# Optimization experiments

Measured on AMD Instinct MI355X. Metric: run time of the kernel, lower is better.

## Reference

```python
import jax, jax.numpy as jnp
import numpy as np
from jax import lax

DIL_R = 2            # dilation_radius
K = 2 * DIL_R + 1    # 5x5 morphology kernel
FOCAL_ALPHA = 0.25
FOCAL_GAMMA = 2.0
BOUNDARY_W = 1.0
IGNORE_IDX = 250


def setup_inputs() -> dict:
    key = jax.random.key(0)
    k1, k2 = jax.random.split(key)
    pred = jax.random.normal(k1, (32, 2, 512, 512), dtype=jnp.float32)
    target = jax.random.randint(k2, (32, 512, 512), 0, 2, dtype=jnp.int64)
    return {"pred": pred, "target": target}


def _boundary_mask(target):
    # labels float, 5x5 all-ones conv with 'same' padding (zero pad),
    # dilated = (conv > 0), eroded = (-conv(-x) > K*K-1) == (conv(x) > K*K-1)
    x = target.astype(jnp.float32)[:, None]                    # [B,1,H,W]
    kern = jnp.ones((1, 1, K, K), dtype=jnp.float32)
    s = lax.conv_general_dilated(x, kern, (1, 1), 'SAME',
                                 dimension_numbers=('NCHW', 'OIHW', 'NCHW'))
    dilated = (s > 0).astype(jnp.float32)
    eroded = (s > (K * K - 1)).astype(jnp.float32)
    return (dilated - eroded)[:, 0]                            # [B,H,W]


def _loss(pred, target, boundary):
    logp = jax.nn.log_softmax(pred, axis=1)                    # [B,2,H,W]
    # per-pixel CE
    ce_pix = -jnp.take_along_axis(logp, target[:, None].astype(jnp.int32), axis=1)[:, 0]  # [B,H,W]
    # main CE with ignore_index=250
    valid = (target != IGNORE_IDX)
    ce_loss = jnp.sum(ce_pix * valid) / jnp.maximum(jnp.sum(valid), 1)
    # focal loss (no ignore, mean over all pixels)
    pt = jnp.exp(-ce_pix)
    focal = jnp.mean(FOCAL_ALPHA * (1.0 - pt) ** FOCAL_GAMMA * ce_pix)
    # boundary dice on class-1 prob
    prob1 = jnp.exp(logp[:, 1])                                # softmax(pred,1)[:,1]
    tgt_f = target.astype(jnp.float32)
    bp = prob1 * boundary
    bt = tgt_f * boundary
    inter = jnp.sum(bp * bt, axis=(1, 2))
    union = jnp.sum(bp, axis=(1, 2)) + jnp.sum(bt, axis=(1, 2))
    dice = 2.0 * inter / (union + 1e-8)
    bdice = 1.0 - jnp.mean(dice)
    return ce_loss + BOUNDARY_W * focal + BOUNDARY_W * bdice


def reference(pred, target):
    boundary = _boundary_mask(target)
    return _loss(pred, target, boundary)
```

## Files before the change

### kernel.cpp

```cpp
#include <hip/hip_runtime.h>
#include <math.h>

#define BATCH 32
#define HH 512
#define WW 512
#define TH 16
#define HALO 2
#define SRH (TH + 2*HALO)
#define NDW (WW / 4)
#define CSTRIDE 132
#define NPIX ((float)BATCH * HH * WW)
#define HW (HH * WW)

#define SLOT(j,b) ((((j) * BATCH) + (b)) * 32)
#define WS_FLOATS (6 * BATCH * 32)

__global__ void zero_ws_kernel(float* ws) {
    int i = blockIdx.x * 256 + threadIdx.x;
    if (i < WS_FLOATS) ws[i] = 0.0f;
}

__global__ __launch_bounds__(256) void bel_main_kernel(
        const float* __restrict__ pred,
        const int*   __restrict__ target,
        float*       __restrict__ ws) {
    __shared__ unsigned int t8[SRH][NDW];
    __shared__ unsigned int csum[TH][CSTRIDE];
    __shared__ float red[6][4];

    const int tid = threadIdx.x;
    const int bid = blockIdx.x;
    const int b   = bid >> 5;
    const int ty  = bid & 31;
    const int y0  = ty * TH;
    const size_t tb = (size_t)b * HW;

    if (tid < 2 * TH) {
        int rr = tid >> 1;
        csum[rr][(tid & 1) ? (NDW + 1) : 0] = 0u;
    }

    #pragma unroll
    for (int it = 0; it < (SRH * NDW) / 256; ++it) {
        const int i  = tid + 256 * it;
        const int r  = i >> 7;
        const int c4 = i & 127;
        const int gy = y0 - HALO + r;
        unsigned int packed = 0u;
        if ((unsigned)gy < (unsigned)HH) {
            const int4 v = *(const int4*)(target + tb + ((size_t)gy << 9) + (c4 << 2));
            packed = (unsigned)v.x | ((unsigned)v.y << 8)
                   | ((unsigned)v.z << 16) | ((unsigned)v.w << 24);
        }
        t8[r][c4] = packed;
    }
    __syncthreads();

    #pragma unroll
    for (int it = 0; it < (TH * NDW) / 256; ++it) {
        const int j = tid + 256 * it;
        const int r = j >> 7;
        const int c = j & 127;
        csum[r][c + 1] = t8[r][c] + t8[r+1][c] + t8[r+2][c]
                       + t8[r+3][c] + t8[r+4][c];
    }
    __syncthreads();

    const float4* __restrict__ pr0 = (const float4*)(pred + tb * 2);
    const float4* __restrict__ pr1 = (const float4*)(pred + tb * 2 + HW);

    float ce_acc = 0.f, cnt_acc = 0.f, focal_acc = 0.f;
    float inter_acc = 0.f, bp_acc = 0.f, bt_acc = 0.f;

    const unsigned long long M5 = 0xFFFFFFFFFFull;
    const unsigned long long ALL5 = 0x0505050505ull;

    for (int it = 0; it < (TH * NDW) / 256; ++it) {
        const int j = tid + 256 * it;
        const int r = j >> 7;
        const int g = j & 127;
        const int y = y0 + r;
        const int fidx = (y << 7) + g;

        const float4 f0 = pr0[fidx];
        const float4 f1 = pr1[fidx];

        const unsigned int L = csum[r][g];
        const unsigned int M = csum[r][g + 1];
        const unsigned int R = csum[r][g + 2];
        const unsigned int tdw = t8[r + HALO][g];

        const unsigned long long lo  = (unsigned long long)L | ((unsigned long long)M << 32);
        const unsigned long long mid = (unsigned long long)M | ((unsigned long long)R << 32);

        #pragma unroll
        for (int i = 0; i < 4; ++i) {
            unsigned long long w;
            if      (i == 0) w = (lo  >> 16) & M5;
            else if (i == 1) w = (lo  >> 24) & M5;
            else if (i == 2) w =  mid        & M5;
            else             w = (mid >>  8) & M5;
            const float bm = (w != 0ull && w != ALL5) ? 1.0f : 0.0f;

            const unsigned int tv = (tdw >> (8 * i)) & 0xFFu;

            const float p0 = (i == 0) ? f0.x : (i == 1) ? f0.y : (i == 2) ? f0.z : f0.w;
            const float p1 = (i == 0) ? f1.x : (i == 1) ? f1.y : (i == 2) ? f1.z : f1.w;

            const float d  = p1 - p0;
            const float e  = __expf(-fabsf(d));
            const float rz = 1.0f / (1.0f + e);
            const float pmin = e * rz;
            const float prob1 = (d >= 0.0f) ? rz : pmin;
            const float pt = tv ? prob1 : (1.0f - prob1);
            const float ce = -__logf(pt);

            const float valid = (tv != 250u) ? 1.0f : 0.0f;
            ce_acc  += ce * valid;
            cnt_acc += valid;

            const float omp = 1.0f - pt;
            focal_acc += omp * omp * ce;

            const float bp = prob1 * bm;
            const float bt = (float)tv * bm;
            inter_acc += bp * bt;
            bp_acc    += bp;
            bt_acc    += bt;
        }
    }

    float vals[6] = {ce_acc, cnt_acc, focal_acc * 0.25f, inter_acc, bp_acc, bt_acc};
    #pragma unroll
    for (int jj = 0; jj < 6; ++jj) {
        float v = vals[jj];
        #pragma unroll
        for (int off = 32; off > 0; off >>= 1)
            v += __shfl_down(v, off, 64);
        vals[jj] = v;
    }
    const int wave = tid >> 6;
    const int lane = tid & 63;
    if (lane == 0) {
        #pragma unroll
        for (int jj = 0; jj < 6; ++jj) red[jj][wave] = vals[jj];
    }
    __syncthreads();
    if (tid == 0) {
        #pragma unroll
        for (int jj = 0; jj < 6; ++jj) {
            const float v = red[jj][0] + red[jj][1] + red[jj][2] + red[jj][3];
            atomicAdd(&ws[SLOT(jj, b)], v);
        }
    }
}

__global__ void bel_finalize_kernel(const float* __restrict__ ws,
                                    float* __restrict__ out) {
    const int t = threadIdx.x;
    float ce_p = 0.f, cnt_p = 0.f, focal_p = 0.f, dice_p = 0.f;
    if (t < BATCH) {
        ce_p    = ws[SLOT(0, t)];
        cnt_p   = ws[SLOT(1, t)];
        focal_p = ws[SLOT(2, t)];
        const float inter = ws[SLOT(3, t)];
        const float uni   = ws[SLOT(4, t)] + ws[SLOT(5, t)];
        dice_p = 2.0f * inter / (uni + 1e-8f);
    }
    #pragma unroll
    for (int off = 32; off > 0; off >>= 1) {
        ce_p    += __shfl_down(ce_p, off, 64);
        cnt_p   += __shfl_down(cnt_p, off, 64);
        focal_p += __shfl_down(focal_p, off, 64);
        dice_p  += __shfl_down(dice_p, off, 64);
    }
    if (t == 0) {
        const float ce_loss = ce_p / fmaxf(cnt_p, 1.0f);
        const float focal   = focal_p / NPIX;
        const float bdice   = 1.0f - dice_p / (float)BATCH;
        out[0] = ce_loss + focal + bdice;
    }
}

extern "C" void kernel_launch(void* const* d_in, const int* in_sizes, int n_in,
                              void* d_out, int out_size, void* d_ws, size_t ws_size,
                              hipStream_t stream) {
    const float* pred   = (const float*)d_in[0];
    const int*   target = (const int*)d_in[1];
    float* ws  = (float*)d_ws;
    float* out = (float*)d_out;

    zero_ws_kernel<<<(WS_FLOATS + 255) / 256, 256, 0, stream>>>(ws);
    bel_main_kernel<<<BATCH * (HH / TH), 256, 0, stream>>>(pred, target, ws);
    bel_finalize_kernel<<<1, 64, 0, stream>>>(ws, out);
}
```

Measured before the change: 118.7 us.

## Prefetch pred tile into registers and replace atomics with per-block partials

```diff
diff --git a/kernel.cpp b/kernel.cpp
--- a/kernel.cpp
+++ b/kernel.cpp
@@ -11,16 +11,10 @@
 #define CSTRIDE 132
 #define NPIX ((float)BATCH * HH * WW)
 #define HW (HH * WW)
-
-#define SLOT(j,b) ((((j) * BATCH) + (b)) * 32)
-#define WS_FLOATS (6 * BATCH * 32)
-
-__global__ void zero_ws_kernel(float* ws) {
-    int i = blockIdx.x * 256 + threadIdx.x;
-    if (i < WS_FLOATS) ws[i] = 0.0f;
-}
-
-__global__ __launch_bounds__(256) void bel_main_kernel(
+#define NBLK (BATCH * (HH / TH))
+
+
+__global__ __launch_bounds__(256, 4) void bel_main_kernel(
         const float* __restrict__ pred,
         const int*   __restrict__ target,
         float*       __restrict__ ws) {
@@ -68,6 +62,13 @@
 
     const float4* __restrict__ pr0 = (const float4*)(pred + tb * 2);
     const float4* __restrict__ pr1 = (const float4*)(pred + tb * 2 + HW);
+    const int base4 = (y0 << 7) + tid;
+
+    float4 F0[8], F1[8];
+    #pragma unroll
+    for (int it = 0; it < 8; ++it) F0[it] = pr0[base4 + 256 * it];
+    #pragma unroll
+    for (int it = 0; it < 8; ++it) F1[it] = pr1[base4 + 256 * it];
 
     float ce_acc = 0.f, cnt_acc = 0.f, focal_acc = 0.f;
     float inter_acc = 0.f, bp_acc = 0.f, bt_acc = 0.f;
@@ -75,15 +76,15 @@
     const unsigned long long M5 = 0xFFFFFFFFFFull;
     const unsigned long long ALL5 = 0x0505050505ull;
 
-    for (int it = 0; it < (TH * NDW) / 256; ++it) {
-        const int j = tid + 256 * it;
-        const int r = j >> 7;
-        const int g = j & 127;
-        const int y = y0 + r;
-        const int fidx = (y << 7) + g;
-
-        const float4 f0 = pr0[fidx];
-        const float4 f1 = pr1[fidx];
+    const int g  = tid & 127;
+    const int rb = tid >> 7;
+
+    #pragma unroll
+    for (int it = 0; it < 8; ++it) {
+        const int r = rb + 2 * it;
+
+        const float4 f0 = F0[it];
+        const float4 f1 = F1[it];
 
         const unsigned int L = csum[r][g];
         const unsigned int M = csum[r][g + 1];
@@ -147,38 +148,62 @@
     }
     __syncthreads();
     if (tid == 0) {
-        #pragma unroll
-        for (int jj = 0; jj < 6; ++jj) {
-            const float v = red[jj][0] + red[jj][1] + red[jj][2] + red[jj][3];
-            atomicAdd(&ws[SLOT(jj, b)], v);
-        }
+        float* p = ws + bid * 8;
+        #pragma unroll
+        for (int jj = 0; jj < 6; ++jj)
+            p[jj] = red[jj][0] + red[jj][1] + red[jj][2] + red[jj][3];
     }
 }
 
 __global__ void bel_finalize_kernel(const float* __restrict__ ws,
                                     float* __restrict__ out) {
+    __shared__ float simg[BATCH][4];
     const int t = threadIdx.x;
-    float ce_p = 0.f, cnt_p = 0.f, focal_p = 0.f, dice_p = 0.f;
+    const int b = t >> 3;
+    const int s = t & 7;
+
+    float a0 = 0.f, a1 = 0.f, a2 = 0.f, a3 = 0.f, a4 = 0.f, a5 = 0.f;
+    #pragma unroll
+    for (int k = 0; k < 4; ++k) {
+        const int bid = (b << 5) + s + (k << 3);
+        const float* p = ws + bid * 8;
+        a0 += p[0]; a1 += p[1]; a2 += p[2];
+        a3 += p[3]; a4 += p[4]; a5 += p[5];
+    }
+    #pragma unroll
+    for (int off = 4; off > 0; off >>= 1) {
+        a0 += __shfl_down(a0, off, 8);
+        a1 += __shfl_down(a1, off, 8);
+        a2 += __shfl_down(a2, off, 8);
+        a3 += __shfl_down(a3, off, 8);
+        a4 += __shfl_down(a4, off, 8);
+        a5 += __shfl_down(a5, off, 8);
+    }
+    if (s == 0) {
+        simg[b][0] = a0;
+        simg[b][1] = a1;
+        simg[b][2] = a2;
+        simg[b][3] = 2.0f * a3 / (a4 + a5 + 1e-8f);
+    }
+    __syncthreads();
     if (t < BATCH) {
-        ce_p    = ws[SLOT(0, t)];
-        cnt_p   = ws[SLOT(1, t)];
-        focal_p = ws[SLOT(2, t)];
-        const float inter = ws[SLOT(3, t)];
-        const float uni   = ws[SLOT(4, t)] + ws[SLOT(5, t)];
-        dice_p = 2.0f * inter / (uni + 1e-8f);
-    }
-    #pragma unroll
-    for (int off = 32; off > 0; off >>= 1) {
-        ce_p    += __shfl_down(ce_p, off, 64);
-        cnt_p   += __shfl_down(cnt_p, off, 64);
-        focal_p += __shfl_down(focal_p, off, 64);
-        dice_p  += __shfl_down(dice_p, off, 64);
-    }
-    if (t == 0) {
-        const float ce_loss = ce_p / fmaxf(cnt_p, 1.0f);
-        const float focal   = focal_p / NPIX;
-        const float bdice   = 1.0f - dice_p / (float)BATCH;
-        out[0] = ce_loss + focal + bdice;
+        float ce  = simg[t][0];
+        float cnt = simg[t][1];
+        float foc = simg[t][2];
+        float dc  = simg[t][3];
+        #pragma unroll
+        for (int off = 16; off > 0; off >>= 1) {
+            ce  += __shfl_down(ce,  off, 32);
+            cnt += __shfl_down(cnt, off, 32);
+            foc += __shfl_down(foc, off, 32);
+            dc  += __shfl_down(dc,  off, 32);
+        }
+        if (t == 0) {
+            const float ce_loss = ce / fmaxf(cnt, 1.0f);
+            const float focal   = foc / NPIX;
+            const float bdice   = 1.0f - dc / (float)BATCH;
+            out[0] = ce_loss + focal + bdice;
+        }
     }
 }
 
@@ -190,7 +215,6 @@
     float* ws  = (float*)d_ws;
     float* out = (float*)d_out;
 
-    zero_ws_kernel<<<(WS_FLOATS + 255) / 256, 256, 0, stream>>>(ws);
-    bel_main_kernel<<<BATCH * (HH / TH), 256, 0, stream>>>(pred, target, ws);
-    bel_finalize_kernel<<<1, 64, 0, stream>>>(ws, out);
+    bel_main_kernel<<<NBLK, 256, 0, stream>>>(pred, target, ws);
+    bel_finalize_kernel<<<1, 256, 0, stream>>>(ws, out);
 }
```

After: 116.7 us. About the same (-1.7%).
